# Optimization experiments

Hardware: AMD Instinct MI355X
Metric: run time of the kernel (lower is better)

Reference implementation:

```python
import jax, jax.numpy as jnp
import numpy as np

N_NODES = 100000
N_EDGES = 1600000
IN_CH, HID_CH, OUT_CH = 128, 64, 64
NEG_SLOPE = 0.2
EPS = 1e-16


def setup_inputs() -> dict:
    key = jax.random.key(0)
    ks = jax.random.split(key, 10)
    x = jax.random.normal(ks[0], (N_NODES, IN_CH), dtype=jnp.float32)
    edge_index = jax.random.randint(ks[1], (2, N_EDGES), 0, N_NODES, dtype=jnp.int64)
    s1 = 1.0 / np.sqrt(IN_CH)
    s2 = 1.0 / np.sqrt(HID_CH)
    return {
        "x": x,
        "edge_index": edge_index,
        "W1": jax.random.normal(ks[2], (IN_CH, HID_CH), dtype=jnp.float32) * s1,
        "a_src1": jax.random.normal(ks[3], (HID_CH,), dtype=jnp.float32) * s2,
        "a_dst1": jax.random.normal(ks[4], (HID_CH,), dtype=jnp.float32) * s2,
        "b1": jnp.zeros((HID_CH,), dtype=jnp.float32),
        "W2": jax.random.normal(ks[5], (HID_CH, OUT_CH), dtype=jnp.float32) * s2,
        "a_src2": jax.random.normal(ks[6], (OUT_CH,), dtype=jnp.float32) * (1.0 / np.sqrt(OUT_CH)),
        "a_dst2": jax.random.normal(ks[7], (OUT_CH,), dtype=jnp.float32) * (1.0 / np.sqrt(OUT_CH)),
        "b2": jnp.zeros((OUT_CH,), dtype=jnp.float32),
    }


def gat_conv(x, src, dst, W, a_s, a_d, b):
    # node projection: [N, d_out]
    h = x @ W
    # per-node attention halves, gathered per edge
    alpha = jax.nn.leaky_relu((h @ a_s)[src] + (h @ a_d)[dst], NEG_SLOPE)  # [E]
    # segment softmax over edges grouped by destination node
    m = jax.ops.segment_max(alpha, dst, num_segments=N_NODES)
    e = jnp.exp(alpha - m[dst])
    z = jax.ops.segment_sum(e, dst, num_segments=N_NODES)
    w = e / (z[dst] + EPS)  # [E]
    # weighted scatter-sum of source features
    out = jax.ops.segment_sum(h[src] * w[:, None], dst, num_segments=N_NODES)
    return out + b


def reference(x, edge_index, W1, a_src1, a_dst1, b1, W2, a_src2, a_dst2, b2):
    # add self loops once (PyG add_self_loops=True in both convs)
    loops = jnp.arange(N_NODES, dtype=edge_index.dtype)
    src = jnp.concatenate([edge_index[0], loops])
    dst = jnp.concatenate([edge_index[1], loops])
    h = jax.nn.relu(gat_conv(x, src, dst, W1, a_src1, a_dst1, b1))
    return gat_conv(h, src, dst, W2, a_src2, a_dst2, b2)
```

## Files before the change

### kernel.cpp

```cpp
#include <hip/hip_runtime.h>
#include <cstdint>

#define NN 100000
#define NX 8
#define NEG 0.2f

__global__ void k_detect(const void* e, int* mode) {
    if (threadIdx.x == 0 && blockIdx.x == 0) {
        const int* p = (const int*)e;
        int allz = 1;
        for (int i = 0; i < 64; ++i)
            if (p[2 * i + 1] != 0) { allz = 0; break; }
        mode[0] = allz;
    }
}

__global__ void k_zero(int* p, int n) {
    int i = blockIdx.x * 256 + threadIdx.x;
    if (i < n) p[i] = 0;
}

__global__ void k_count(const void* e, long E, const int* mode, int* cnt) {
    long i = (long)blockIdx.x * 256 + threadIdx.x;
    if (i >= E) return;
    const int x = (int)(blockIdx.x & (NX - 1));
    long d;
    if (mode[0]) d = (long)((const long long*)e)[E + i];
    else         d = ((const int*)e)[E + i];
    atomicAdd(&cnt[(long)x * NN + d], 1);
}

__global__ void k_scan_block(const int* cnt, int* S, int* bsums, int n) {
    __shared__ int sm[256];
    int i = blockIdx.x * 256 + threadIdx.x;
    int v = (i < n) ? cnt[i] : 0;
    sm[threadIdx.x] = v;
    __syncthreads();
    for (int off = 1; off < 256; off <<= 1) {
        int t = (threadIdx.x >= off) ? sm[threadIdx.x - off] : 0;
        __syncthreads();
        sm[threadIdx.x] += t;
        __syncthreads();
    }
    if (i < n) S[i] = sm[threadIdx.x] - v;
    if (threadIdx.x == 255) bsums[blockIdx.x] = sm[255];
}

__global__ void k_scan_mid(int* bs, int nb) {
    __shared__ int sm[1024];
    __shared__ int carry_s;
    const int t = threadIdx.x;
    if (t == 0) carry_s = 0;
    __syncthreads();
    for (int r = 0; r * 1024 < nb; ++r) {
        int i = r * 1024 + t;
        int v = (i < nb) ? bs[i] : 0;
        sm[t] = v;
        __syncthreads();
        for (int off = 1; off < 1024; off <<= 1) {
            int tv = (t >= off) ? sm[t - off] : 0;
            __syncthreads();
            sm[t] += tv;
            __syncthreads();
        }
        int carry = carry_s;
        if (i < nb) bs[i] = sm[t] - v + carry;
        __syncthreads();
        if (t == 1023) carry_s = carry + sm[1023];
        __syncthreads();
    }
}

__global__ void k_scan_add(int* S, const int* bsums, int n) {
    int i = blockIdx.x * 256 + threadIdx.x;
    if (i < n) S[i] += bsums[blockIdx.x];
}

__global__ void k_fill(const void* e, long E, const int* mode, int* S, int* csr) {
    long i = (long)blockIdx.x * 256 + threadIdx.x;
    if (i >= E) return;
    const int x = (int)(blockIdx.x & (NX - 1));
    long s, d;
    if (mode[0]) {
        const long long* p = (const long long*)e;
        s = (long)p[i]; d = (long)p[E + i];
    } else {
        const int* p = (const int*)e;
        s = p[i]; d = p[E + i];
    }
    int pos = atomicAdd(&S[(long)x * NN + d], 1);
    csr[pos] = (int)s;
}

template <int K>
__global__ __launch_bounds__(256) void k_gemm_attn(
    const float* __restrict__ X, const float* __restrict__ W,
    const float* __restrict__ As, const float* __restrict__ Ad,
    float* __restrict__ H, float* __restrict__ AS, float* __restrict__ AD, int n) {
    constexpr int KC = 32;
    __shared__ float Wl[KC * 64];
    __shared__ float Xt[KC][68];
    const int tid = threadIdx.x;
    const int tx = tid & 15, ty = tid >> 4;
    const long row0 = (long)blockIdx.x * 64;
    float acc[4][4] = {{0.f}};

    for (int k0 = 0; k0 < K; k0 += KC) {
        __syncthreads();
        {
            const float4* src = (const float4*)(W + (long)k0 * 64);
            float4* dst = (float4*)Wl;
            for (int i = tid; i < KC * 64 / 4; i += 256) dst[i] = src[i];
        }
        {
            const int rr = tid >> 3;
            const int kq = tid & 7;
#pragma unroll
            for (int h = 0; h < 2; ++h) {
                int r = rr + h * 32;
                long row = row0 + r;
                if (row >= n) row = n - 1;
                float4 v = *(const float4*)(X + row * K + k0 + kq * 4);
                Xt[kq * 4 + 0][r] = v.x;
                Xt[kq * 4 + 1][r] = v.y;
                Xt[kq * 4 + 2][r] = v.z;
                Xt[kq * 4 + 3][r] = v.w;
            }
        }
        __syncthreads();
#pragma unroll
        for (int kk = 0; kk < KC; ++kk) {
            float4 xv = *(const float4*)(&Xt[kk][ty * 4]);
            float4 wv = *(const float4*)(&Wl[kk * 64 + tx * 4]);
            acc[0][0] += xv.x * wv.x; acc[0][1] += xv.x * wv.y;
            acc[0][2] += xv.x * wv.z; acc[0][3] += xv.x * wv.w;
            acc[1][0] += xv.y * wv.x; acc[1][1] += xv.y * wv.y;
            acc[1][2] += xv.y * wv.z; acc[1][3] += xv.y * wv.w;
            acc[2][0] += xv.z * wv.x; acc[2][1] += xv.z * wv.y;
            acc[2][2] += xv.z * wv.z; acc[2][3] += xv.z * wv.w;
            acc[3][0] += xv.w * wv.x; acc[3][1] += xv.w * wv.y;
            acc[3][2] += xv.w * wv.z; acc[3][3] += xv.w * wv.w;
        }
    }

#pragma unroll
    for (int i = 0; i < 4; ++i) {
        long row = row0 + ty * 4 + i;
        if (row < n) {
            float4 o = {acc[i][0], acc[i][1], acc[i][2], acc[i][3]};
            *(float4*)(H + row * 64 + tx * 4) = o;
        }
    }
    float4 asv = *(const float4*)(As + tx * 4);
    float4 adv = *(const float4*)(Ad + tx * 4);
#pragma unroll
    for (int i = 0; i < 4; ++i) {
        float ps = acc[i][0] * asv.x + acc[i][1] * asv.y + acc[i][2] * asv.z + acc[i][3] * asv.w;
        float pd = acc[i][0] * adv.x + acc[i][1] * adv.y + acc[i][2] * adv.z + acc[i][3] * adv.w;
#pragma unroll
        for (int off = 1; off < 16; off <<= 1) {
            ps += __shfl_xor(ps, off);
            pd += __shfl_xor(pd, off);
        }
        if (tx == 0) {
            long row = row0 + ty * 4 + i;
            if (row < n) { AS[row] = ps; AD[row] = pd; }
        }
    }
}

__global__ __launch_bounds__(256) void k_agg(
    const int* __restrict__ cnt, const int* __restrict__ S,
    const int* __restrict__ csr,
    const float* __restrict__ AS, const float* __restrict__ AD,
    const float* __restrict__ H, const float* __restrict__ B,
    float* __restrict__ OUT, int n, int relu) {
    const int lane = threadIdx.x & 63;
    const int node = blockIdx.x * 4 + (threadIdx.x >> 6);
    if (node >= n) return;

    int cx[NX], sx[NX];
#pragma unroll
    for (int x = 0; x < NX; ++x) {
        int c = cnt[x * NN + node];
        int en = S[x * NN + node];
        cx[x] = c;
        sx[x] = en - c;
    }
    int degI = 0;
#pragma unroll
    for (int x = 0; x < NX; ++x) degI += cx[x];
    const int degT = degI + 1;
    const float ad = AD[node];

    auto lookup = [&](int e) -> int {
        if (e >= degI) return node;
        int addr = 0, cum = 0;
#pragma unroll
        for (int x = 0; x < NX; ++x) {
            int o = e - cum;
            if (o >= 0 && o < cx[x]) addr = sx[x] + o;
            cum += cx[x];
        }
        return csr[addr];
    };

    float acc = 0.f;
    if (degT <= 64) {
        const bool v = lane < degT;
        int s = lookup(lane);
        float a = v ? AS[s] + ad : -__builtin_inff();
        a = (a >= 0.f) ? a : NEG * a;
        float m = a;
#pragma unroll
        for (int off = 32; off; off >>= 1) m = fmaxf(m, __shfl_xor(m, off));
        float ez = v ? __expf(a - m) : 0.f;
        float z = ez;
#pragma unroll
        for (int off = 32; off; off >>= 1) z += __shfl_xor(z, off);
        float wgt = ez * (1.f / (z + 1e-16f));
        int j = 0;
        for (; j + 4 <= degT; j += 4) {
            int s0 = __shfl(s, j), s1 = __shfl(s, j + 1);
            int s2 = __shfl(s, j + 2), s3 = __shfl(s, j + 3);
            float w0 = __shfl(wgt, j), w1 = __shfl(wgt, j + 1);
            float w2 = __shfl(wgt, j + 2), w3 = __shfl(wgt, j + 3);
            float h0 = H[(long)s0 * 64 + lane];
            float h1 = H[(long)s1 * 64 + lane];
            float h2 = H[(long)s2 * 64 + lane];
            float h3 = H[(long)s3 * 64 + lane];
            acc += w0 * h0 + w1 * h1 + w2 * h2 + w3 * h3;
        }
        for (; j < degT; ++j) {
            int sj = __shfl(s, j);
            float wj = __shfl(wgt, j);
            acc += wj * H[(long)sj * 64 + lane];
        }
    } else {
        float m = -__builtin_inff(), z = 0.f;
        for (int p0 = 0; p0 < degT; p0 += 64) {
            int e = p0 + lane;
            bool v = e < degT;
            int s = lookup(e);
            float a = v ? AS[s] + ad : -__builtin_inff();
            a = (a >= 0.f) ? a : NEG * a;
            float cm = a;
#pragma unroll
            for (int off = 32; off; off >>= 1) cm = fmaxf(cm, __shfl_xor(cm, off));
            float mn = fmaxf(m, cm);
            float ez = v ? __expf(a - mn) : 0.f;
#pragma unroll
            for (int off = 32; off; off >>= 1) ez += __shfl_xor(ez, off);
            z = (p0 == 0) ? ez : z * __expf(m - mn) + ez;
            m = mn;
        }
        const float invz = 1.f / (z + 1e-16f);
        for (int p0 = 0; p0 < degT; p0 += 64) {
            int e = p0 + lane;
            bool v = e < degT;
            int s = lookup(e);
            float wgt = 0.f;
            if (v) {
                float a = AS[s] + ad;
                a = (a >= 0.f) ? a : NEG * a;
                wgt = __expf(a - m) * invz;
            }
            int cntv = min(64, degT - p0);
            for (int j = 0; j < cntv; ++j) {
                int sj = __shfl(s, j);
                float wj = __shfl(wgt, j);
                acc += wj * H[(long)sj * 64 + lane];
            }
        }
    }
    acc += B[lane];
    if (relu) acc = fmaxf(acc, 0.f);
    OUT[(long)node * 64 + lane] = acc;
}

extern "C" void kernel_launch(void* const* d_in, const int* in_sizes, int n_in,
                              void* d_out, int out_size, void* d_ws, size_t ws_size,
                              hipStream_t stream) {
    const float* x   = (const float*)d_in[0];
    const void*  eix = d_in[1];
    const float* W1  = (const float*)d_in[2];
    const float* as1 = (const float*)d_in[3];
    const float* ad1 = (const float*)d_in[4];
    const float* b1  = (const float*)d_in[5];
    const float* W2  = (const float*)d_in[6];
    const float* as2 = (const float*)d_in[7];
    const float* ad2 = (const float*)d_in[8];
    const float* b2  = (const float*)d_in[9];
    float* out = (float*)d_out;

    const int  n  = NN;
    const long E  = (long)in_sizes[1] / 2;
    const int  NS = NX * NN;

    char* w = (char*)d_ws;
    size_t off = 0;
    auto alloc = [&](size_t bytes) -> void* {
        void* p = w + off;
        off = (off + bytes + 255) & ~(size_t)255;
        return p;
    };
    int*   mode  = (int*)alloc(4);
    int*   cnt   = (int*)alloc((size_t)NS * 4);
    int*   S     = (int*)alloc((size_t)NS * 4);
    int*   bsums = (int*)alloc(4096 * 4);
    int*   csr   = (int*)alloc((size_t)E * 4);
    float* H     = (float*)alloc((size_t)n * 64 * 4);
    float* AS    = (float*)alloc((size_t)n * 4);
    float* AD    = (float*)alloc((size_t)n * 4);

    const int nbS = (NS + 255) / 256;
    const int nbE = (int)((E + 255) / 256);
    const int nbG = (n + 63) / 64;

    k_detect<<<1, 64, 0, stream>>>(eix, mode);
    k_zero<<<nbS, 256, 0, stream>>>(cnt, NS);
    k_count<<<nbE, 256, 0, stream>>>(eix, E, mode, cnt);
    k_scan_block<<<nbS, 256, 0, stream>>>(cnt, S, bsums, NS);
    k_scan_mid<<<1, 1024, 0, stream>>>(bsums, nbS);
    k_scan_add<<<nbS, 256, 0, stream>>>(S, bsums, NS);
    k_fill<<<nbE, 256, 0, stream>>>(eix, E, mode, S, csr);

    k_gemm_attn<128><<<nbG, 256, 0, stream>>>(x, W1, as1, ad1, H, AS, AD, n);
    k_agg<<<(n + 3) / 4, 256, 0, stream>>>(cnt, S, csr, AS, AD, H, b1, out, n, 1);
    k_gemm_attn<64><<<nbG, 256, 0, stream>>>(out, W2, as2, ad2, H, AS, AD, n);
    k_agg<<<(n + 3) / 4, 256, 0, stream>>>(cnt, S, csr, AS, AD, H, b2, out, n, 0);
}
```

Before: 463.1 us.

## Compact sharded CSR into contiguous per-node rows and unroll gather by eight

Adds a reorder kernel that merges the eight sharded CSR slices into one contiguous per-destination CSR with a row pointer array. The aggregation kernels then read a single beg/end pair and index directly instead of loading 16 counters per node and running an 8-way lookup per edge. The gather loop is also unrolled from 4 to 8 neighbour loads for more memory-level parallelism. The cost is an extra pass over the edge list, using a serial per-thread copy, plus another E-sized buffer.

```diff
diff --git a/kernel.cpp b/kernel.cpp
--- a/kernel.cpp
+++ b/kernel.cpp
@@ -90,6 +90,33 @@
     }
     int pos = atomicAdd(&S[(long)x * NN + d], 1);
     csr[pos] = (int)s;
+}
+
+__global__ void k_reorder(const int* cnt, const int* Send, const int* csr,
+                          int* csr2, int* rowptr2, long E, int n) {
+    int d = blockIdx.x * 256 + threadIdx.x;
+    if (d >= n) return;
+    int C = 0, sum = 0;
+    int st[NX], cx[NX];
+#pragma unroll
+    for (int x = 0; x < NX; ++x) {
+        int c0 = cnt[(long)x * NN];
+        int e0 = Send[(long)x * NN];
+        C += e0 - c0;
+        int c = cnt[(long)x * NN + d];
+        int en = Send[(long)x * NN + d];
+        cx[x] = c;
+        st[x] = en - c;
+        sum += en - c;
+    }
+    int start = sum - C;
+    rowptr2[d] = start;
+    if (d == 0) rowptr2[n] = (int)E;
+#pragma unroll
+    for (int x = 0; x < NX; ++x) {
+        int c = cx[x], s0 = st[x];
+        for (int j = 0; j < c; ++j) csr2[start++] = csr[s0 + j];
+    }
 }
 
 template <int K>
@@ -170,45 +197,22 @@
 }
 
 __global__ __launch_bounds__(256) void k_agg(
-    const int* __restrict__ cnt, const int* __restrict__ S,
-    const int* __restrict__ csr,
+    const int* __restrict__ rowptr, const int* __restrict__ csr,
     const float* __restrict__ AS, const float* __restrict__ AD,
     const float* __restrict__ H, const float* __restrict__ B,
     float* __restrict__ OUT, int n, int relu) {
     const int lane = threadIdx.x & 63;
     const int node = blockIdx.x * 4 + (threadIdx.x >> 6);
     if (node >= n) return;
-
-    int cx[NX], sx[NX];
-#pragma unroll
-    for (int x = 0; x < NX; ++x) {
-        int c = cnt[x * NN + node];
-        int en = S[x * NN + node];
-        cx[x] = c;
-        sx[x] = en - c;
-    }
-    int degI = 0;
-#pragma unroll
-    for (int x = 0; x < NX; ++x) degI += cx[x];
+    const int beg = rowptr[node], end = rowptr[node + 1];
+    const int degI = end - beg;
     const int degT = degI + 1;
     const float ad = AD[node];
-
-    auto lookup = [&](int e) -> int {
-        if (e >= degI) return node;
-        int addr = 0, cum = 0;
-#pragma unroll
-        for (int x = 0; x < NX; ++x) {
-            int o = e - cum;
-            if (o >= 0 && o < cx[x]) addr = sx[x] + o;
-            cum += cx[x];
-        }
-        return csr[addr];
-    };
 
     float acc = 0.f;
     if (degT <= 64) {
         const bool v = lane < degT;
-        int s = lookup(lane);
+        int s = (lane < degI) ? csr[beg + lane] : node;
         float a = v ? AS[s] + ad : -__builtin_inff();
         a = (a >= 0.f) ? a : NEG * a;
         float m = a;
@@ -220,16 +224,25 @@
         for (int off = 32; off; off >>= 1) z += __shfl_xor(z, off);
         float wgt = ez * (1.f / (z + 1e-16f));
         int j = 0;
-        for (; j + 4 <= degT; j += 4) {
-            int s0 = __shfl(s, j), s1 = __shfl(s, j + 1);
+        for (; j + 8 <= degT; j += 8) {
+            int s0 = __shfl(s, j),     s1 = __shfl(s, j + 1);
             int s2 = __shfl(s, j + 2), s3 = __shfl(s, j + 3);
-            float w0 = __shfl(wgt, j), w1 = __shfl(wgt, j + 1);
+            int s4 = __shfl(s, j + 4), s5 = __shfl(s, j + 5);
+            int s6 = __shfl(s, j + 6), s7 = __shfl(s, j + 7);
+            float w0 = __shfl(wgt, j),     w1 = __shfl(wgt, j + 1);
             float w2 = __shfl(wgt, j + 2), w3 = __shfl(wgt, j + 3);
+            float w4 = __shfl(wgt, j + 4), w5 = __shfl(wgt, j + 5);
+            float w6 = __shfl(wgt, j + 6), w7 = __shfl(wgt, j + 7);
             float h0 = H[(long)s0 * 64 + lane];
             float h1 = H[(long)s1 * 64 + lane];
             float h2 = H[(long)s2 * 64 + lane];
             float h3 = H[(long)s3 * 64 + lane];
+            float h4 = H[(long)s4 * 64 + lane];
+            float h5 = H[(long)s5 * 64 + lane];
+            float h6 = H[(long)s6 * 64 + lane];
+            float h7 = H[(long)s7 * 64 + lane];
             acc += w0 * h0 + w1 * h1 + w2 * h2 + w3 * h3;
+            acc += w4 * h4 + w5 * h5 + w6 * h6 + w7 * h7;
         }
         for (; j < degT; ++j) {
             int sj = __shfl(s, j);
@@ -241,7 +254,7 @@
         for (int p0 = 0; p0 < degT; p0 += 64) {
             int e = p0 + lane;
             bool v = e < degT;
-            int s = lookup(e);
+            int s = (e < degI) ? csr[beg + e] : node;
             float a = v ? AS[s] + ad : -__builtin_inff();
             a = (a >= 0.f) ? a : NEG * a;
             float cm = a;
@@ -258,7 +271,7 @@
         for (int p0 = 0; p0 < degT; p0 += 64) {
             int e = p0 + lane;
             bool v = e < degT;
-            int s = lookup(e);
+            int s = (e < degI) ? csr[beg + e] : node;
             float wgt = 0.f;
             if (v) {
                 float a = AS[s] + ad;
@@ -304,17 +317,20 @@
         off = (off + bytes + 255) & ~(size_t)255;
         return p;
     };
-    int*   mode  = (int*)alloc(4);
-    int*   cnt   = (int*)alloc((size_t)NS * 4);
-    int*   S     = (int*)alloc((size_t)NS * 4);
-    int*   bsums = (int*)alloc(4096 * 4);
-    int*   csr   = (int*)alloc((size_t)E * 4);
-    float* H     = (float*)alloc((size_t)n * 64 * 4);
-    float* AS    = (float*)alloc((size_t)n * 4);
-    float* AD    = (float*)alloc((size_t)n * 4);
+    int*   mode    = (int*)alloc(4);
+    int*   cnt     = (int*)alloc((size_t)NS * 4);
+    int*   S       = (int*)alloc((size_t)NS * 4);
+    int*   bsums   = (int*)alloc(4096 * 4);
+    int*   csr     = (int*)alloc((size_t)E * 4);
+    int*   csr2    = (int*)alloc((size_t)E * 4);
+    int*   rowptr2 = (int*)alloc((size_t)(n + 1) * 4);
+    float* H       = (float*)alloc((size_t)n * 64 * 4);
+    float* AS      = (float*)alloc((size_t)n * 4);
+    float* AD      = (float*)alloc((size_t)n * 4);
 
     const int nbS = (NS + 255) / 256;
     const int nbE = (int)((E + 255) / 256);
+    const int nbN = (n + 255) / 256;
     const int nbG = (n + 63) / 64;
 
     k_detect<<<1, 64, 0, stream>>>(eix, mode);
@@ -324,9 +340,10 @@
     k_scan_mid<<<1, 1024, 0, stream>>>(bsums, nbS);
     k_scan_add<<<nbS, 256, 0, stream>>>(S, bsums, NS);
     k_fill<<<nbE, 256, 0, stream>>>(eix, E, mode, S, csr);
+    k_reorder<<<nbN, 256, 0, stream>>>(cnt, S, csr, csr2, rowptr2, E, n);
 
     k_gemm_attn<128><<<nbG, 256, 0, stream>>>(x, W1, as1, ad1, H, AS, AD, n);
-    k_agg<<<(n + 3) / 4, 256, 0, stream>>>(cnt, S, csr, AS, AD, H, b1, out, n, 1);
+    k_agg<<<(n + 3) / 4, 256, 0, stream>>>(rowptr2, csr2, AS, AD, H, b1, out, n, 1);
     k_gemm_attn<64><<<nbG, 256, 0, stream>>>(out, W2, as2, ad2, H, AS, AD, n);
-    k_agg<<<(n + 3) / 4, 256, 0, stream>>>(cnt, S, csr, AS, AD, H, b2, out, n, 0);
-}
+    k_agg<<<(n + 3) / 4, 256, 0, stream>>>(rowptr2, csr2, AS, AD, H, b2, out, n, 0);
+}
```

Result: no change. 461.2 us (-0.4%).
